# Kernel tuning notes

Measured on AMD Instinct MI355X. Metric: run time of the kernel, lower is better.

Reference implementation:

```python
import jax, jax.numpy as jnp
import numpy as np

M, B, S, D, H = 8, 4, 512, 512, 8
HD = D // H  # head_dim = 64


def setup_inputs() -> dict:
    key = jax.random.key(0)
    k1, k2, k3 = jax.random.split(key, 3)
    x = jax.random.normal(k1, (M, B, S, D), dtype=jnp.float32)
    qkv_weight = jax.random.normal(k2, (M, D, 3 * D), dtype=jnp.float32) * 0.02
    proj_weight = jax.random.normal(k3, (M, D, D), dtype=jnp.float32) * 0.02
    return {"x": x, "qkv_weight": qkv_weight, "proj_weight": proj_weight}


def reference(x, qkv_weight, proj_weight):
    m, b, s, d = x.shape
    # model-axis batched QKV projection
    qkv = jnp.einsum('mbti,mio->mbto', x, qkv_weight)
    q, k, v = jnp.split(qkv, 3, axis=-1)
    # [m, b, h, s, hd]
    q = q.reshape(m, b, s, H, HD).transpose(0, 1, 3, 2, 4)
    k = k.reshape(m, b, s, H, HD).transpose(0, 1, 3, 2, 4)
    v = v.reshape(m, b, s, H, HD).transpose(0, 1, 3, 2, 4)
    att = jnp.einsum('mbhqd,mbhkd->mbhqk', q, k) / jnp.sqrt(jnp.float32(HD))
    causal = jnp.tril(jnp.ones((s, s), dtype=bool))
    att = jnp.where(causal, att, jnp.float32(-jnp.inf))
    att = jax.nn.softmax(att, axis=-1)
    y = jnp.einsum('mbhqk,mbhkd->mbhqd', att, v)
    y = y.transpose(0, 1, 3, 2, 4).reshape(m, b, s, d)
    return jnp.einsum('mbti,mio->mbto', y, proj_weight)
```

## Files before the change

kernel.cpp:

```cpp
#include <hip/hip_runtime.h>
#include <hip/hip_bf16.h>


typedef unsigned short u16;
typedef unsigned int u32;
typedef __attribute__((ext_vector_type(8))) short short8;
typedef __attribute__((ext_vector_type(4))) float f32x4;
typedef __attribute__((ext_vector_type(4))) unsigned short u16x4;
typedef __attribute__((ext_vector_type(8))) unsigned short u16x8;
typedef __attribute__((ext_vector_type(2))) unsigned int u32x2;

#define MFMA16(a, b, c) __builtin_amdgcn_mfma_f32_16x16x32_bf16((a), (b), (c), 0, 0, 0)

__device__ __forceinline__ u16 f2bf(float f) {
  union { __hip_bfloat16 h; u16 u; } cv;
  cv.h = __float2bfloat16(f);
  return cv.u;
}

__device__ __forceinline__ void gl_lds16(const u16* g, u16* l) {
  __builtin_amdgcn_global_load_lds(
      (const __attribute__((address_space(1))) void*)g,
      (__attribute__((address_space(3))) void*)l, 16, 0, 0);
}

__global__ __launch_bounds__(256) void xcast_kernel(const float* __restrict__ in,
                                                    u16* __restrict__ out, long n8) {
  long stride = (long)gridDim.x * 256;
  for (long i = blockIdx.x * 256L + threadIdx.x; i < n8; i += stride) {
    f32x4 a = *(const f32x4*)(in + i * 8);
    f32x4 b = *(const f32x4*)(in + i * 8 + 4);
    u16x8 o = {f2bf(a[0]), f2bf(a[1]), f2bf(a[2]), f2bf(a[3]),
               f2bf(b[0]), f2bf(b[1]), f2bf(b[2]), f2bf(b[3])};
    *(u16x8*)(out + i * 8) = o;
  }
}

__global__ __launch_bounds__(256) void wtrans_kernel(const float* __restrict__ in,
                                                     u16* __restrict__ out, int R, int C) {
  __shared__ float t[32][33];
  int m = blockIdx.z;
  const float* pin = in + (size_t)m * R * C;
  u16* pout = out + (size_t)m * R * C;
  int c0 = blockIdx.x * 32, r0 = blockIdx.y * 32;
  int tx = threadIdx.x, ty = threadIdx.y;
#pragma unroll
  for (int i = 0; i < 4; ++i) {
    int r = ty + i * 8;
    t[r][tx] = pin[(size_t)(r0 + r) * C + c0 + tx];
  }
  __syncthreads();
#pragma unroll
  for (int i = 0; i < 4; ++i) {
    int r = ty + i * 8;
    pout[(size_t)(c0 + r) * R + r0 + tx] = f2bf(t[tx][r]);
  }
}

__global__ __launch_bounds__(256) void qkv_gemm_kernel(const u16* __restrict__ XB,
                                                       const u16* __restrict__ WT,
                                                       u16* __restrict__ Q,
                                                       u16* __restrict__ K,
                                                       u16* __restrict__ VT) {
  __shared__ __attribute__((aligned(16))) u16 As[3][128 * 32];
  __shared__ __attribute__((aligned(16))) u16 Bs[3][128 * 32];
  int bid = blockIdx.x;
  int wgid = (bid & 7) * 192 + (bid >> 3);
  int m = wgid / 192;
  int rem = wgid % 192;
  int r0 = (rem / 12) * 128, c0 = (rem % 12) * 128;
  const u16* A = XB + (size_t)m * 2048 * 512;
  const u16* BT = WT + (size_t)m * 1536 * 512;
  int t = threadIdx.x;
  int lane = t & 63, w = t >> 6;
  int wr = (w >> 1) * 64, wc = (w & 1) * 64;
  int fr = lane & 15, fc = lane >> 4;

  int rA0 = t >> 2, cA0 = t & 3, sA0 = cA0 ^ ((rA0 >> 1) & 3);
  int rA1 = (t + 256) >> 2, cA1 = t & 3, sA1 = cA1 ^ ((rA1 >> 1) & 3);

  f32x4 acc[4][4];
#pragma unroll
  for (int i = 0; i < 4; ++i)
#pragma unroll
    for (int j = 0; j < 4; ++j) acc[i][j] = f32x4{0.f, 0.f, 0.f, 0.f};

#define QKV_STAGE(tile)                                                          \
  {                                                                              \
    int kk_ = (tile) * 32;                                                       \
    int b_ = (tile) % 3;                                                         \
    gl_lds16(A + (size_t)(r0 + rA0) * 512 + kk_ + sA0 * 8, &As[b_][w * 512]);    \
    gl_lds16(A + (size_t)(r0 + rA1) * 512 + kk_ + sA1 * 8, &As[b_][2048 + w * 512]); \
    gl_lds16(BT + (size_t)(c0 + rA0) * 512 + kk_ + sA0 * 8, &Bs[b_][w * 512]);   \
    gl_lds16(BT + (size_t)(c0 + rA1) * 512 + kk_ + sA1 * 8, &Bs[b_][2048 + w * 512]); \
  }

#define QKV_COMPUTE(tile)                                                        \
  {                                                                              \
    int b_ = (tile) % 3;                                                         \
    short8 af[4], bf_[4];                                                        \
    _Pragma("unroll") for (int i = 0; i < 4; ++i) {                              \
      int row = wr + i * 16 + fr;                                                \
      int sl = fc ^ ((row >> 1) & 3);                                            \
      af[i] = *(const short8*)&As[b_][row * 32 + sl * 8];                        \
    }                                                                            \
    _Pragma("unroll") for (int j = 0; j < 4; ++j) {                              \
      int row = wc + j * 16 + fr;                                                \
      int sl = fc ^ ((row >> 1) & 3);                                            \
      bf_[j] = *(const short8*)&Bs[b_][row * 32 + sl * 8];                       \
    }                                                                            \
    _Pragma("unroll") for (int i = 0; i < 4; ++i)                                \
      _Pragma("unroll") for (int j = 0; j < 4; ++j)                              \
        acc[i][j] = MFMA16(af[i], bf_[j], acc[i][j]);                            \
  }

  QKV_STAGE(0);
  QKV_STAGE(1);
  for (int ks = 0; ks < 14; ++ks) {
    asm volatile("s_waitcnt vmcnt(4)" ::: "memory");
    __builtin_amdgcn_sched_barrier(0);
    __builtin_amdgcn_s_barrier();
    QKV_STAGE(ks + 2);
    QKV_COMPUTE(ks);
    __builtin_amdgcn_sched_barrier(0);
  }
  asm volatile("s_waitcnt vmcnt(0)" ::: "memory");
  __builtin_amdgcn_sched_barrier(0);
  __builtin_amdgcn_s_barrier();
  QKV_COMPUTE(14);
  QKV_COMPUTE(15);

  int seg = c0 >> 9;
  if (seg == 2) {
#pragma unroll
    for (int i = 0; i < 4; ++i)
#pragma unroll
      for (int j = 0; j < 4; ++j) {
        int s0 = r0 + wr + i * 16 + fc * 4;
        int gcol = c0 + wc + j * 16 + fr;
        int cc = gcol & 511;
        int hh = cc >> 6, hd = cc & 63;
        int b = s0 >> 9, s = s0 & 511;
        size_t headoff = (size_t)((m * 4 + b) * 8 + hh) * 32768;
        u16x4 pk = {f2bf(acc[i][j][0]), f2bf(acc[i][j][1]),
                    f2bf(acc[i][j][2]), f2bf(acc[i][j][3])};
        *(u16x4*)(VT + headoff + (size_t)hd * 512 + s) = pk;
      }
  } else {
#pragma unroll
    for (int i = 0; i < 4; ++i)
#pragma unroll
      for (int j = 0; j < 4; ++j)
#pragma unroll
        for (int r = 0; r < 4; ++r) {
          int grow = r0 + wr + i * 16 + fc * 4 + r;
          int gcol = c0 + wc + j * 16 + fr;
          int b = grow >> 9, s = grow & 511;
          int cc = gcol & 511;
          int hh = cc >> 6, hd = cc & 63;
          size_t headoff = (size_t)((m * 4 + b) * 8 + hh) * 32768;
          u16 val = f2bf(acc[i][j][r]);
          if (seg == 0) Q[headoff + s * 64 + hd] = val;
          else          K[headoff + s * 64 + hd] = val;
        }
  }
}

__global__ __launch_bounds__(256) void attn_kernel(const u16* __restrict__ Qg,
                                                   const u16* __restrict__ Kg,
                                                   const u16* __restrict__ VTg,
                                                   u16* __restrict__ Yg) {
  __shared__ u16 Ks[2][64][72];
  __shared__ u16 Vs[2][64][72];
  __shared__ u16 Pl[4][16][72];
  int bid = blockIdx.x;
  int qt = bid >> 8;
  int g = bid & 255;
  int h = g & 7, mb = g >> 3;
  int t = threadIdx.x, lane = t & 63, w = t >> 6;
  int fr = lane & 15, fc = lane >> 4;
  size_t hoff = ((size_t)mb * 8 + h) * 32768;
  const u16* Q = Qg + hoff;
  const u16* K = Kg + hoff;
  const u16* V = VTg + hoff;
  int qrow = qt * 64 + w * 16 + fr;
  const float SC = 0.125f * 1.44269504088896340736f;

  short8 qf0 = *(const short8*)(Q + (size_t)qrow * 64 + fc * 8);
  short8 qf1 = *(const short8*)(Q + (size_t)qrow * 64 + 32 + fc * 8);

  f32x4 acc[4];
#pragma unroll
  for (int d = 0; d < 4; ++d) acc[d] = f32x4{0.f, 0.f, 0.f, 0.f};
  float mst = -1e30f, lst = 0.f;

  int u0 = 2 * t, u1 = 2 * t + 1;
  int kr0 = u0 >> 3, kc0 = (u0 & 7) * 8;
  int kr1 = u1 >> 3, kc1 = (u1 & 7) * 8;

  {
    u16x8 a0 = *(const u16x8*)(K + (size_t)kr0 * 64 + kc0);
    u16x8 a1 = *(const u16x8*)(K + (size_t)kr1 * 64 + kc1);
    u16x8 b0 = *(const u16x8*)(V + (size_t)kr0 * 512 + kc0);
    u16x8 b1 = *(const u16x8*)(V + (size_t)kr1 * 512 + kc1);
    *(u16x8*)&Ks[0][kr0][kc0] = a0;
    *(u16x8*)&Ks[0][kr1][kc1] = a1;
    *(u16x8*)&Vs[0][kr0][kc0] = b0;
    *(u16x8*)&Vs[0][kr1][kc1] = b1;
  }
  __syncthreads();

  for (int kt = 0; kt <= qt; ++kt) {
    int cur = kt & 1;
    bool pref = kt < qt;
    u16x8 nk0, nk1, nv0, nv1;
    if (pref) {
      int kbn = (kt + 1) * 64;
      nk0 = *(const u16x8*)(K + (size_t)(kbn + kr0) * 64 + kc0);
      nk1 = *(const u16x8*)(K + (size_t)(kbn + kr1) * 64 + kc1);
      nv0 = *(const u16x8*)(V + (size_t)kr0 * 512 + kbn + kc0);
      nv1 = *(const u16x8*)(V + (size_t)kr1 * 512 + kbn + kc1);
    }

    f32x4 st[4];
#pragma unroll
    for (int sub = 0; sub < 4; ++sub) {
      short8 kf0 = *(const short8*)&Ks[cur][sub * 16 + fr][fc * 8];
      short8 kf1 = *(const short8*)&Ks[cur][sub * 16 + fr][32 + fc * 8];
      f32x4 z = f32x4{0.f, 0.f, 0.f, 0.f};
      z = MFMA16(kf0, qf0, z);
      st[sub] = MFMA16(kf1, qf1, z);
    }

    float p[4][4];
    float mt = -3e30f;
    bool diag = (kt == qt);
    int qloc = w * 16 + fr;
#pragma unroll
    for (int sub = 0; sub < 4; ++sub)
#pragma unroll
      for (int r = 0; r < 4; ++r) {
        float v = st[sub][r] * SC;
        if (diag && (sub * 16 + fc * 4 + r) > qloc) v = -1e30f;
        p[sub][r] = v;
        mt = fmaxf(mt, v);
      }
    mt = fmaxf(mt, __shfl_xor(mt, 16));
    mt = fmaxf(mt, __shfl_xor(mt, 32));
    float mn = fmaxf(mst, mt);
    float al = __builtin_amdgcn_exp2f(mst - mn);
    mst = mn;
    float rs = 0.f;
#pragma unroll
    for (int sub = 0; sub < 4; ++sub)
#pragma unroll
      for (int r = 0; r < 4; ++r) {
        float e = __builtin_amdgcn_exp2f(p[sub][r] - mn);
        p[sub][r] = e;
        rs += e;
      }
    rs += __shfl_xor(rs, 16);
    rs += __shfl_xor(rs, 32);
    lst = lst * al + rs;
#pragma unroll
    for (int d = 0; d < 4; ++d) acc[d] *= al;

#pragma unroll
    for (int sub = 0; sub < 4; ++sub) {
      u32 lo = (u32)f2bf(p[sub][0]) | ((u32)f2bf(p[sub][1]) << 16);
      u32 hi = (u32)f2bf(p[sub][2]) | ((u32)f2bf(p[sub][3]) << 16);
      *(u32x2*)&Pl[w][fr][sub * 16 + fc * 4] = u32x2{lo, hi};
    }

#pragma unroll
    for (int dt = 0; dt < 4; ++dt)
#pragma unroll
      for (int kc = 0; kc < 2; ++kc) {
        short8 vf = *(const short8*)&Vs[cur][dt * 16 + fr][kc * 32 + fc * 8];
        short8 pb = *(const short8*)&Pl[w][fr][kc * 32 + fc * 8];
        acc[dt] = MFMA16(vf, pb, acc[dt]);
      }

    if (pref) {
      *(u16x8*)&Ks[cur ^ 1][kr0][kc0] = nk0;
      *(u16x8*)&Ks[cur ^ 1][kr1][kc1] = nk1;
      *(u16x8*)&Vs[cur ^ 1][kr0][kc0] = nv0;
      *(u16x8*)&Vs[cur ^ 1][kr1][kc1] = nv1;
    }
    __syncthreads();
  }

  float inv = 1.0f / lst;
#pragma unroll
  for (int dt = 0; dt < 4; ++dt) {
    u16x4 o = {f2bf(acc[dt][0] * inv), f2bf(acc[dt][1] * inv),
               f2bf(acc[dt][2] * inv), f2bf(acc[dt][3] * inv)};
    *(u16x4*)(Yg + ((size_t)mb * 512 + qrow) * 512 + h * 64 + dt * 16 + fc * 4) = o;
  }
}

__global__ __launch_bounds__(256) void proj_gemm_kernel(const u16* __restrict__ Y,
                                                        const u16* __restrict__ PT,
                                                        float* __restrict__ OUT) {
  __shared__ __attribute__((aligned(16))) u16 As[3][128 * 32];
  __shared__ __attribute__((aligned(16))) u16 Bs[3][128 * 32];
  int bid = blockIdx.x;
  int wgid = (bid & 7) * 64 + (bid >> 3);
  int m = wgid / 64;
  int rem = wgid % 64;
  int r0 = (rem / 4) * 128, c0 = (rem % 4) * 128;
  const u16* A = Y + (size_t)m * 2048 * 512;
  const u16* BT = PT + (size_t)m * 512 * 512;
  float* C = OUT + (size_t)m * 2048 * 512;
  int t = threadIdx.x;
  int lane = t & 63, w = t >> 6;
  int wr = (w >> 1) * 64, wc = (w & 1) * 64;
  int fr = lane & 15, fc = lane >> 4;

  int rA0 = t >> 2, sA0 = (t & 3) ^ ((rA0 >> 1) & 3);
  int rA1 = (t + 256) >> 2, sA1 = (t & 3) ^ ((rA1 >> 1) & 3);

  f32x4 acc[4][4];
#pragma unroll
  for (int i = 0; i < 4; ++i)
#pragma unroll
    for (int j = 0; j < 4; ++j) acc[i][j] = f32x4{0.f, 0.f, 0.f, 0.f};

#define PROJ_STAGE(tile)                                                         \
  {                                                                              \
    int kk_ = (tile) * 32;                                                       \
    int b_ = (tile) % 3;                                                         \
    gl_lds16(A + (size_t)(r0 + rA0) * 512 + kk_ + sA0 * 8, &As[b_][w * 512]);    \
    gl_lds16(A + (size_t)(r0 + rA1) * 512 + kk_ + sA1 * 8, &As[b_][2048 + w * 512]); \
    gl_lds16(BT + (size_t)(c0 + rA0) * 512 + kk_ + sA0 * 8, &Bs[b_][w * 512]);   \
    gl_lds16(BT + (size_t)(c0 + rA1) * 512 + kk_ + sA1 * 8, &Bs[b_][2048 + w * 512]); \
  }

#define PROJ_COMPUTE(tile)                                                       \
  {                                                                              \
    int b_ = (tile) % 3;                                                         \
    short8 af[4], bf_[4];                                                        \
    _Pragma("unroll") for (int i = 0; i < 4; ++i) {                              \
      int row = wr + i * 16 + fr;                                                \
      int sl = fc ^ ((row >> 1) & 3);                                            \
      af[i] = *(const short8*)&As[b_][row * 32 + sl * 8];                        \
    }                                                                            \
    _Pragma("unroll") for (int j = 0; j < 4; ++j) {                              \
      int row = wc + j * 16 + fr;                                                \
      int sl = fc ^ ((row >> 1) & 3);                                            \
      bf_[j] = *(const short8*)&Bs[b_][row * 32 + sl * 8];                       \
    }                                                                            \
    _Pragma("unroll") for (int i = 0; i < 4; ++i)                                \
      _Pragma("unroll") for (int j = 0; j < 4; ++j)                              \
        acc[i][j] = MFMA16(af[i], bf_[j], acc[i][j]);                            \
  }

  PROJ_STAGE(0);
  PROJ_STAGE(1);
  for (int ks = 0; ks < 14; ++ks) {
    asm volatile("s_waitcnt vmcnt(4)" ::: "memory");
    __builtin_amdgcn_sched_barrier(0);
    __builtin_amdgcn_s_barrier();
    PROJ_STAGE(ks + 2);
    PROJ_COMPUTE(ks);
    __builtin_amdgcn_sched_barrier(0);
  }
  asm volatile("s_waitcnt vmcnt(0)" ::: "memory");
  __builtin_amdgcn_sched_barrier(0);
  __builtin_amdgcn_s_barrier();
  PROJ_COMPUTE(14);
  PROJ_COMPUTE(15);

#pragma unroll
  for (int i = 0; i < 4; ++i)
#pragma unroll
    for (int j = 0; j < 4; ++j)
#pragma unroll
      for (int r = 0; r < 4; ++r) {
        int grow = r0 + wr + i * 16 + fc * 4 + r;
        int gcol = c0 + wc + j * 16 + fr;
        C[(size_t)grow * 512 + gcol] = acc[i][j][r];
      }
}

extern "C" void kernel_launch(void* const* d_in, const int* in_sizes, int n_in,
                              void* d_out, int out_size, void* d_ws, size_t ws_size,
                              hipStream_t stream) {
  const float* x = (const float*)d_in[0];
  const float* wqkv = (const float*)d_in[1];
  const float* wproj = (const float*)d_in[2];
  float* out = (float*)d_out;

  u16* p = (u16*)d_ws;
  u16* wqkvT = p;  p += (size_t)8 * 1536 * 512;
  u16* wprojT = p; p += (size_t)8 * 512 * 512;
  u16* qb = p;     p += (size_t)8388608;
  u16* kb = p;     p += (size_t)8388608;
  u16* vtb = p;    p += (size_t)8388608;
  u16* xyb = p;    p += (size_t)8388608;

  xcast_kernel<<<2048, 256, 0, stream>>>(x, xyb, (long)8 * 4 * 512 * 512 / 8);
  wtrans_kernel<<<dim3(48, 16, 8), dim3(32, 8), 0, stream>>>(wqkv, wqkvT, 512, 1536);
  wtrans_kernel<<<dim3(16, 16, 8), dim3(32, 8), 0, stream>>>(wproj, wprojT, 512, 512);
  qkv_gemm_kernel<<<1536, 256, 0, stream>>>(xyb, wqkvT, qb, kb, vtb);
  attn_kernel<<<2048, 256, 0, stream>>>(qb, kb, vtb, xyb);
  proj_gemm_kernel<<<512, 256, 0, stream>>>(xyb, wprojT, out);
}
```

Baseline: 191.5 us.

## Enlarge GEMM tiles to 256x128 and pair causal query tiles in attention

Both GEMM kernels now run 512-thread workgroups, each computing a 256x128 output tile, so every B tile loaded is reused across twice as many rows and fewer blocks are launched. The attention kernel pairs query tile p with tile 7-p in one block to balance causal work, and shares each K/V tile load between the two. K/V staging now uses asynchronous global-to-LDS loads into an XOR-swizzled layout in place of register round-trips. The trade-off is more registers and LDS per block, which may lower occupancy, and each attention block runs a longer serial loop.

```diff
diff --git a/kernel.cpp b/kernel.cpp
--- a/kernel.cpp
+++ b/kernel.cpp
@@ -57,18 +57,18 @@
   }
 }
 
-__global__ __launch_bounds__(256) void qkv_gemm_kernel(const u16* __restrict__ XB,
+__global__ __launch_bounds__(512) void qkv_gemm_kernel(const u16* __restrict__ XB,
                                                        const u16* __restrict__ WT,
                                                        u16* __restrict__ Q,
                                                        u16* __restrict__ K,
                                                        u16* __restrict__ VT) {
-  __shared__ __attribute__((aligned(16))) u16 As[3][128 * 32];
+  __shared__ __attribute__((aligned(16))) u16 As[3][256 * 32];
   __shared__ __attribute__((aligned(16))) u16 Bs[3][128 * 32];
   int bid = blockIdx.x;
-  int wgid = (bid & 7) * 192 + (bid >> 3);
-  int m = wgid / 192;
-  int rem = wgid % 192;
-  int r0 = (rem / 12) * 128, c0 = (rem % 12) * 128;
+  int wgid = (bid & 7) * 96 + (bid >> 3);
+  int m = wgid / 96;
+  int rem = wgid % 96;
+  int r0 = (rem / 12) * 256, c0 = (rem % 12) * 128;
   const u16* A = XB + (size_t)m * 2048 * 512;
   const u16* BT = WT + (size_t)m * 1536 * 512;
   int t = threadIdx.x;
@@ -76,8 +76,8 @@
   int wr = (w >> 1) * 64, wc = (w & 1) * 64;
   int fr = lane & 15, fc = lane >> 4;
 
-  int rA0 = t >> 2, cA0 = t & 3, sA0 = cA0 ^ ((rA0 >> 1) & 3);
-  int rA1 = (t + 256) >> 2, cA1 = t & 3, sA1 = cA1 ^ ((rA1 >> 1) & 3);
+  int rA0 = t >> 2, sA0 = (t & 3) ^ ((rA0 >> 1) & 3);
+  int rA1 = 128 + (t >> 2), sA1 = (t & 3) ^ ((rA1 >> 1) & 3);
 
   f32x4 acc[4][4];
 #pragma unroll
@@ -85,39 +85,38 @@
 #pragma unroll
     for (int j = 0; j < 4; ++j) acc[i][j] = f32x4{0.f, 0.f, 0.f, 0.f};
 
-#define QKV_STAGE(tile)                                                          \
-  {                                                                              \
-    int kk_ = (tile) * 32;                                                       \
-    int b_ = (tile) % 3;                                                         \
-    gl_lds16(A + (size_t)(r0 + rA0) * 512 + kk_ + sA0 * 8, &As[b_][w * 512]);    \
-    gl_lds16(A + (size_t)(r0 + rA1) * 512 + kk_ + sA1 * 8, &As[b_][2048 + w * 512]); \
-    gl_lds16(BT + (size_t)(c0 + rA0) * 512 + kk_ + sA0 * 8, &Bs[b_][w * 512]);   \
-    gl_lds16(BT + (size_t)(c0 + rA1) * 512 + kk_ + sA1 * 8, &Bs[b_][2048 + w * 512]); \
-  }
-
-#define QKV_COMPUTE(tile)                                                        \
-  {                                                                              \
-    int b_ = (tile) % 3;                                                         \
-    short8 af[4], bf_[4];                                                        \
-    _Pragma("unroll") for (int i = 0; i < 4; ++i) {                              \
-      int row = wr + i * 16 + fr;                                                \
-      int sl = fc ^ ((row >> 1) & 3);                                            \
-      af[i] = *(const short8*)&As[b_][row * 32 + sl * 8];                        \
-    }                                                                            \
-    _Pragma("unroll") for (int j = 0; j < 4; ++j) {                              \
-      int row = wc + j * 16 + fr;                                                \
-      int sl = fc ^ ((row >> 1) & 3);                                            \
-      bf_[j] = *(const short8*)&Bs[b_][row * 32 + sl * 8];                       \
-    }                                                                            \
-    _Pragma("unroll") for (int i = 0; i < 4; ++i)                                \
-      _Pragma("unroll") for (int j = 0; j < 4; ++j)                              \
-        acc[i][j] = MFMA16(af[i], bf_[j], acc[i][j]);                            \
+#define QKV_STAGE(tile)                                                            \
+  {                                                                                \
+    int kk_ = (tile) * 32;                                                         \
+    int b_ = (tile) % 3;                                                           \
+    gl_lds16(A + (size_t)(r0 + rA0) * 512 + kk_ + sA0 * 8, &As[b_][w * 512]);      \
+    gl_lds16(A + (size_t)(r0 + rA1) * 512 + kk_ + sA1 * 8, &As[b_][4096 + w * 512]); \
+    gl_lds16(BT + (size_t)(c0 + rA0) * 512 + kk_ + sA0 * 8, &Bs[b_][w * 512]);     \
+  }
+
+#define QKV_COMPUTE(tile)                                                          \
+  {                                                                                \
+    int b_ = (tile) % 3;                                                           \
+    short8 af[4], bf_[4];                                                          \
+    _Pragma("unroll") for (int i = 0; i < 4; ++i) {                                \
+      int row = wr + i * 16 + fr;                                                  \
+      int sl = fc ^ ((row >> 1) & 3);                                              \
+      af[i] = *(const short8*)&As[b_][row * 32 + sl * 8];                          \
+    }                                                                              \
+    _Pragma("unroll") for (int j = 0; j < 4; ++j) {                                \
+      int row = wc + j * 16 + fr;                                                  \
+      int sl = fc ^ ((row >> 1) & 3);                                              \
+      bf_[j] = *(const short8*)&Bs[b_][row * 32 + sl * 8];                         \
+    }                                                                              \
+    _Pragma("unroll") for (int i = 0; i < 4; ++i)                                  \
+      _Pragma("unroll") for (int j = 0; j < 4; ++j)                                \
+        acc[i][j] = MFMA16(af[i], bf_[j], acc[i][j]);                              \
   }
 
   QKV_STAGE(0);
   QKV_STAGE(1);
   for (int ks = 0; ks < 14; ++ks) {
-    asm volatile("s_waitcnt vmcnt(4)" ::: "memory");
+    asm volatile("s_waitcnt vmcnt(3)" ::: "memory");
     __builtin_amdgcn_sched_barrier(0);
     __builtin_amdgcn_s_barrier();
     QKV_STAGE(ks + 2);
@@ -170,145 +169,153 @@
                                                    const u16* __restrict__ Kg,
                                                    const u16* __restrict__ VTg,
                                                    u16* __restrict__ Yg) {
-  __shared__ u16 Ks[2][64][72];
-  __shared__ u16 Vs[2][64][72];
+  __shared__ __attribute__((aligned(16))) u16 Ks[2][64 * 64];
+  __shared__ __attribute__((aligned(16))) u16 Vs[2][64 * 64];
   __shared__ u16 Pl[4][16][72];
   int bid = blockIdx.x;
-  int qt = bid >> 8;
+  int p = bid >> 8;
   int g = bid & 255;
   int h = g & 7, mb = g >> 3;
+  int qtA = p, qtB = 7 - p;
   int t = threadIdx.x, lane = t & 63, w = t >> 6;
   int fr = lane & 15, fc = lane >> 4;
   size_t hoff = ((size_t)mb * 8 + h) * 32768;
   const u16* Q = Qg + hoff;
   const u16* K = Kg + hoff;
   const u16* V = VTg + hoff;
-  int qrow = qt * 64 + w * 16 + fr;
   const float SC = 0.125f * 1.44269504088896340736f;
 
-  short8 qf0 = *(const short8*)(Q + (size_t)qrow * 64 + fc * 8);
-  short8 qf1 = *(const short8*)(Q + (size_t)qrow * 64 + 32 + fc * 8);
-
-  f32x4 acc[4];
-#pragma unroll
-  for (int d = 0; d < 4; ++d) acc[d] = f32x4{0.f, 0.f, 0.f, 0.f};
-  float mst = -1e30f, lst = 0.f;
-
-  int u0 = 2 * t, u1 = 2 * t + 1;
-  int kr0 = u0 >> 3, kc0 = (u0 & 7) * 8;
-  int kr1 = u1 >> 3, kc1 = (u1 & 7) * 8;
-
-  {
-    u16x8 a0 = *(const u16x8*)(K + (size_t)kr0 * 64 + kc0);
-    u16x8 a1 = *(const u16x8*)(K + (size_t)kr1 * 64 + kc1);
-    u16x8 b0 = *(const u16x8*)(V + (size_t)kr0 * 512 + kc0);
-    u16x8 b1 = *(const u16x8*)(V + (size_t)kr1 * 512 + kc1);
-    *(u16x8*)&Ks[0][kr0][kc0] = a0;
-    *(u16x8*)&Ks[0][kr1][kc1] = a1;
-    *(u16x8*)&Vs[0][kr0][kc0] = b0;
-    *(u16x8*)&Vs[0][kr1][kc1] = b1;
-  }
-  __syncthreads();
-
-  for (int kt = 0; kt <= qt; ++kt) {
+  int qrowA = qtA * 64 + w * 16 + fr;
+  int qrowB = qtB * 64 + w * 16 + fr;
+  short8 qA0 = *(const short8*)(Q + (size_t)qrowA * 64 + fc * 8);
+  short8 qA1 = *(const short8*)(Q + (size_t)qrowA * 64 + 32 + fc * 8);
+  short8 qB0 = *(const short8*)(Q + (size_t)qrowB * 64 + fc * 8);
+  short8 qB1 = *(const short8*)(Q + (size_t)qrowB * 64 + 32 + fc * 8);
+
+  f32x4 accA[4], accB[4];
+#pragma unroll
+  for (int d = 0; d < 4; ++d) {
+    accA[d] = f32x4{0.f, 0.f, 0.f, 0.f};
+    accB[d] = f32x4{0.f, 0.f, 0.f, 0.f};
+  }
+  float mstA = -1e30f, lstA = 0.f, mstB = -1e30f, lstB = 0.f;
+
+  int sr0 = t >> 3, ss0 = (t & 7) ^ (sr0 & 7);
+  int sr1 = 32 + (t >> 3), ss1 = (t & 7) ^ (sr1 & 7);
+
+#define ATTN_STAGE(kt_, buf_)                                                     \
+  {                                                                               \
+    int kb_ = (kt_) * 64;                                                         \
+    gl_lds16(K + (size_t)(kb_ + sr0) * 64 + ss0 * 8, &Ks[buf_][w * 512]);         \
+    gl_lds16(K + (size_t)(kb_ + sr1) * 64 + ss1 * 8, &Ks[buf_][2048 + w * 512]);  \
+    gl_lds16(V + (size_t)sr0 * 512 + kb_ + ss0 * 8, &Vs[buf_][w * 512]);          \
+    gl_lds16(V + (size_t)sr1 * 512 + kb_ + ss1 * 8, &Vs[buf_][2048 + w * 512]);   \
+  }
+
+  int qloc = w * 16 + fr;
+  ATTN_STAGE(0, 0);
+
+  for (int kt = 0; kt <= qtB; ++kt) {
     int cur = kt & 1;
-    bool pref = kt < qt;
-    u16x8 nk0, nk1, nv0, nv1;
-    if (pref) {
-      int kbn = (kt + 1) * 64;
-      nk0 = *(const u16x8*)(K + (size_t)(kbn + kr0) * 64 + kc0);
-      nk1 = *(const u16x8*)(K + (size_t)(kbn + kr1) * 64 + kc1);
-      nv0 = *(const u16x8*)(V + (size_t)kr0 * 512 + kbn + kc0);
-      nv1 = *(const u16x8*)(V + (size_t)kr1 * 512 + kbn + kc1);
+    if (kt < qtB) {
+      ATTN_STAGE(kt + 1, cur ^ 1);
+      asm volatile("s_waitcnt vmcnt(4)" ::: "memory");
+    } else {
+      asm volatile("s_waitcnt vmcnt(0)" ::: "memory");
     }
-
-    f32x4 st[4];
-#pragma unroll
-    for (int sub = 0; sub < 4; ++sub) {
-      short8 kf0 = *(const short8*)&Ks[cur][sub * 16 + fr][fc * 8];
-      short8 kf1 = *(const short8*)&Ks[cur][sub * 16 + fr][32 + fc * 8];
-      f32x4 z = f32x4{0.f, 0.f, 0.f, 0.f};
-      z = MFMA16(kf0, qf0, z);
-      st[sub] = MFMA16(kf1, qf1, z);
-    }
-
-    float p[4][4];
-    float mt = -3e30f;
-    bool diag = (kt == qt);
-    int qloc = w * 16 + fr;
-#pragma unroll
-    for (int sub = 0; sub < 4; ++sub)
-#pragma unroll
-      for (int r = 0; r < 4; ++r) {
-        float v = st[sub][r] * SC;
-        if (diag && (sub * 16 + fc * 4 + r) > qloc) v = -1e30f;
-        p[sub][r] = v;
-        mt = fmaxf(mt, v);
+    __builtin_amdgcn_sched_barrier(0);
+    __builtin_amdgcn_s_barrier();
+
+    auto tile_compute = [&](const short8& qf0, const short8& qf1, f32x4(&acc)[4],
+                            float& mst, float& lst, bool diag) {
+      f32x4 st[4];
+#pragma unroll
+      for (int sub = 0; sub < 4; ++sub) {
+        int row = sub * 16 + fr;
+        short8 kf0 = *(const short8*)&Ks[cur][row * 64 + ((fc ^ (row & 7)) & 7) * 8];
+        short8 kf1 = *(const short8*)&Ks[cur][row * 64 + (((4 + fc) ^ (row & 7)) & 7) * 8];
+        f32x4 z = f32x4{0.f, 0.f, 0.f, 0.f};
+        z = MFMA16(kf0, qf0, z);
+        st[sub] = MFMA16(kf1, qf1, z);
       }
-    mt = fmaxf(mt, __shfl_xor(mt, 16));
-    mt = fmaxf(mt, __shfl_xor(mt, 32));
-    float mn = fmaxf(mst, mt);
-    float al = __builtin_amdgcn_exp2f(mst - mn);
-    mst = mn;
-    float rs = 0.f;
-#pragma unroll
-    for (int sub = 0; sub < 4; ++sub)
-#pragma unroll
-      for (int r = 0; r < 4; ++r) {
-        float e = __builtin_amdgcn_exp2f(p[sub][r] - mn);
-        p[sub][r] = e;
-        rs += e;
+      float pv[4][4];
+      float mt = -3e30f;
+#pragma unroll
+      for (int sub = 0; sub < 4; ++sub)
+#pragma unroll
+        for (int r = 0; r < 4; ++r) {
+          float v = st[sub][r] * SC;
+          if (diag && (sub * 16 + fc * 4 + r) > qloc) v = -1e30f;
+          pv[sub][r] = v;
+          mt = fmaxf(mt, v);
+        }
+      mt = fmaxf(mt, __shfl_xor(mt, 16));
+      mt = fmaxf(mt, __shfl_xor(mt, 32));
+      float mn = fmaxf(mst, mt);
+      float al = __builtin_amdgcn_exp2f(mst - mn);
+      mst = mn;
+      float rs = 0.f;
+#pragma unroll
+      for (int sub = 0; sub < 4; ++sub)
+#pragma unroll
+        for (int r = 0; r < 4; ++r) {
+          float e = __builtin_amdgcn_exp2f(pv[sub][r] - mn);
+          pv[sub][r] = e;
+          rs += e;
+        }
+      rs += __shfl_xor(rs, 16);
+      rs += __shfl_xor(rs, 32);
+      lst = lst * al + rs;
+#pragma unroll
+      for (int d = 0; d < 4; ++d) acc[d] *= al;
+
+#pragma unroll
+      for (int sub = 0; sub < 4; ++sub) {
+        u32 lo = (u32)f2bf(pv[sub][0]) | ((u32)f2bf(pv[sub][1]) << 16);
+        u32 hi = (u32)f2bf(pv[sub][2]) | ((u32)f2bf(pv[sub][3]) << 16);
+        *(u32x2*)&Pl[w][fr][sub * 16 + fc * 4] = u32x2{lo, hi};
       }
-    rs += __shfl_xor(rs, 16);
-    rs += __shfl_xor(rs, 32);
-    lst = lst * al + rs;
-#pragma unroll
-    for (int d = 0; d < 4; ++d) acc[d] *= al;
-
-#pragma unroll
-    for (int sub = 0; sub < 4; ++sub) {
-      u32 lo = (u32)f2bf(p[sub][0]) | ((u32)f2bf(p[sub][1]) << 16);
-      u32 hi = (u32)f2bf(p[sub][2]) | ((u32)f2bf(p[sub][3]) << 16);
-      *(u32x2*)&Pl[w][fr][sub * 16 + fc * 4] = u32x2{lo, hi};
-    }
-
-#pragma unroll
-    for (int dt = 0; dt < 4; ++dt)
-#pragma unroll
-      for (int kc = 0; kc < 2; ++kc) {
-        short8 vf = *(const short8*)&Vs[cur][dt * 16 + fr][kc * 32 + fc * 8];
-        short8 pb = *(const short8*)&Pl[w][fr][kc * 32 + fc * 8];
-        acc[dt] = MFMA16(vf, pb, acc[dt]);
-      }
-
-    if (pref) {
-      *(u16x8*)&Ks[cur ^ 1][kr0][kc0] = nk0;
-      *(u16x8*)&Ks[cur ^ 1][kr1][kc1] = nk1;
-      *(u16x8*)&Vs[cur ^ 1][kr0][kc0] = nv0;
-      *(u16x8*)&Vs[cur ^ 1][kr1][kc1] = nv1;
-    }
-    __syncthreads();
-  }
-
-  float inv = 1.0f / lst;
+#pragma unroll
+      for (int dt = 0; dt < 4; ++dt)
+#pragma unroll
+        for (int kc = 0; kc < 2; ++kc) {
+          int row = dt * 16 + fr;
+          short8 vf = *(const short8*)&Vs[cur][row * 64 + (((kc * 4 + fc) ^ (row & 7)) & 7) * 8];
+          short8 pb = *(const short8*)&Pl[w][fr][kc * 32 + fc * 8];
+          acc[dt] = MFMA16(vf, pb, acc[dt]);
+        }
+    };
+
+    if (kt <= qtA) tile_compute(qA0, qA1, accA, mstA, lstA, kt == qtA);
+    tile_compute(qB0, qB1, accB, mstB, lstB, kt == qtB);
+
+    asm volatile("s_waitcnt lgkmcnt(0)" ::: "memory");
+    __builtin_amdgcn_sched_barrier(0);
+    __builtin_amdgcn_s_barrier();
+  }
+
+  float invA = 1.0f / lstA, invB = 1.0f / lstB;
 #pragma unroll
   for (int dt = 0; dt < 4; ++dt) {
-    u16x4 o = {f2bf(acc[dt][0] * inv), f2bf(acc[dt][1] * inv),
-               f2bf(acc[dt][2] * inv), f2bf(acc[dt][3] * inv)};
-    *(u16x4*)(Yg + ((size_t)mb * 512 + qrow) * 512 + h * 64 + dt * 16 + fc * 4) = o;
-  }
-}
-
-__global__ __launch_bounds__(256) void proj_gemm_kernel(const u16* __restrict__ Y,
+    u16x4 oA = {f2bf(accA[dt][0] * invA), f2bf(accA[dt][1] * invA),
+                f2bf(accA[dt][2] * invA), f2bf(accA[dt][3] * invA)};
+    *(u16x4*)(Yg + ((size_t)mb * 512 + qrowA) * 512 + h * 64 + dt * 16 + fc * 4) = oA;
+    u16x4 oB = {f2bf(accB[dt][0] * invB), f2bf(accB[dt][1] * invB),
+                f2bf(accB[dt][2] * invB), f2bf(accB[dt][3] * invB)};
+    *(u16x4*)(Yg + ((size_t)mb * 512 + qrowB) * 512 + h * 64 + dt * 16 + fc * 4) = oB;
+  }
+}
+
+__global__ __launch_bounds__(512) void proj_gemm_kernel(const u16* __restrict__ Y,
                                                         const u16* __restrict__ PT,
                                                         float* __restrict__ OUT) {
-  __shared__ __attribute__((aligned(16))) u16 As[3][128 * 32];
+  __shared__ __attribute__((aligned(16))) u16 As[3][256 * 32];
   __shared__ __attribute__((aligned(16))) u16 Bs[3][128 * 32];
   int bid = blockIdx.x;
-  int wgid = (bid & 7) * 64 + (bid >> 3);
-  int m = wgid / 64;
-  int rem = wgid % 64;
-  int r0 = (rem / 4) * 128, c0 = (rem % 4) * 128;
+  int wgid = (bid & 7) * 32 + (bid >> 3);
+  int m = wgid / 32;
+  int rem = wgid % 32;
+  int r0 = (rem / 4) * 256, c0 = (rem % 4) * 128;
   const u16* A = Y + (size_t)m * 2048 * 512;
   const u16* BT = PT + (size_t)m * 512 * 512;
   float* C = OUT + (size_t)m * 2048 * 512;
@@ -318,7 +325,7 @@
   int fr = lane & 15, fc = lane >> 4;
 
   int rA0 = t >> 2, sA0 = (t & 3) ^ ((rA0 >> 1) & 3);
-  int rA1 = (t + 256) >> 2, sA1 = (t & 3) ^ ((rA1 >> 1) & 3);
+  int rA1 = 128 + (t >> 2), sA1 = (t & 3) ^ ((rA1 >> 1) & 3);
 
   f32x4 acc[4][4];
 #pragma unroll
@@ -326,39 +333,38 @@
 #pragma unroll
     for (int j = 0; j < 4; ++j) acc[i][j] = f32x4{0.f, 0.f, 0.f, 0.f};
 
-#define PROJ_STAGE(tile)                                                         \
-  {                                                                              \
-    int kk_ = (tile) * 32;                                                       \
-    int b_ = (tile) % 3;                                                         \
-    gl_lds16(A + (size_t)(r0 + rA0) * 512 + kk_ + sA0 * 8, &As[b_][w * 512]);    \
-    gl_lds16(A + (size_t)(r0 + rA1) * 512 + kk_ + sA1 * 8, &As[b_][2048 + w * 512]); \
-    gl_lds16(BT + (size_t)(c0 + rA0) * 512 + kk_ + sA0 * 8, &Bs[b_][w * 512]);   \
-    gl_lds16(BT + (size_t)(c0 + rA1) * 512 + kk_ + sA1 * 8, &Bs[b_][2048 + w * 512]); \
-  }
-
-#define PROJ_COMPUTE(tile)                                                       \
-  {                                                                              \
-    int b_ = (tile) % 3;                                                         \
-    short8 af[4], bf_[4];                                                        \
-    _Pragma("unroll") for (int i = 0; i < 4; ++i) {                              \
-      int row = wr + i * 16 + fr;                                                \
-      int sl = fc ^ ((row >> 1) & 3);                                            \
-      af[i] = *(const short8*)&As[b_][row * 32 + sl * 8];                        \
-    }                                                                            \
-    _Pragma("unroll") for (int j = 0; j < 4; ++j) {                              \
-      int row = wc + j * 16 + fr;                                                \
-      int sl = fc ^ ((row >> 1) & 3);                                            \
-      bf_[j] = *(const short8*)&Bs[b_][row * 32 + sl * 8];                       \
-    }                                                                            \
-    _Pragma("unroll") for (int i = 0; i < 4; ++i)                                \
-      _Pragma("unroll") for (int j = 0; j < 4; ++j)                              \
-        acc[i][j] = MFMA16(af[i], bf_[j], acc[i][j]);                            \
+#define PROJ_STAGE(tile)                                                           \
+  {                                                                                \
+    int kk_ = (tile) * 32;                                                         \
+    int b_ = (tile) % 3;                                                           \
+    gl_lds16(A + (size_t)(r0 + rA0) * 512 + kk_ + sA0 * 8, &As[b_][w * 512]);      \
+    gl_lds16(A + (size_t)(r0 + rA1) * 512 + kk_ + sA1 * 8, &As[b_][4096 + w * 512]); \
+    gl_lds16(BT + (size_t)(c0 + rA0) * 512 + kk_ + sA0 * 8, &Bs[b_][w * 512]);     \
+  }
+
+#define PROJ_COMPUTE(tile)                                                         \
+  {                                                                                \
+    int b_ = (tile) % 3;                                                           \
+    short8 af[4], bf_[4];                                                          \
+    _Pragma("unroll") for (int i = 0; i < 4; ++i) {                                \
+      int row = wr + i * 16 + fr;                                                  \
+      int sl = fc ^ ((row >> 1) & 3);                                              \
+      af[i] = *(const short8*)&As[b_][row * 32 + sl * 8];                          \
+    }                                                                              \
+    _Pragma("unroll") for (int j = 0; j < 4; ++j) {                                \
+      int row = wc + j * 16 + fr;                                                  \
+      int sl = fc ^ ((row >> 1) & 3);                                              \
+      bf_[j] = *(const short8*)&Bs[b_][row * 32 + sl * 8];                         \
+    }                                                                              \
+    _Pragma("unroll") for (int i = 0; i < 4; ++i)                                  \
+      _Pragma("unroll") for (int j = 0; j < 4; ++j)                                \
+        acc[i][j] = MFMA16(af[i], bf_[j], acc[i][j]);                              \
   }
 
   PROJ_STAGE(0);
   PROJ_STAGE(1);
   for (int ks = 0; ks < 14; ++ks) {
-    asm volatile("s_waitcnt vmcnt(4)" ::: "memory");
+    asm volatile("s_waitcnt vmcnt(3)" ::: "memory");
     __builtin_amdgcn_sched_barrier(0);
     __builtin_amdgcn_s_barrier();
     PROJ_STAGE(ks + 2);
@@ -402,7 +408,7 @@
   xcast_kernel<<<2048, 256, 0, stream>>>(x, xyb, (long)8 * 4 * 512 * 512 / 8);
   wtrans_kernel<<<dim3(48, 16, 8), dim3(32, 8), 0, stream>>>(wqkv, wqkvT, 512, 1536);
   wtrans_kernel<<<dim3(16, 16, 8), dim3(32, 8), 0, stream>>>(wproj, wprojT, 512, 512);
-  qkv_gemm_kernel<<<1536, 256, 0, stream>>>(xyb, wqkvT, qb, kb, vtb);
-  attn_kernel<<<2048, 256, 0, stream>>>(qb, kb, vtb, xyb);
-  proj_gemm_kernel<<<512, 256, 0, stream>>>(xyb, wprojT, out);
-}
+  qkv_gemm_kernel<<<768, 512, 0, stream>>>(xyb, wqkvT, qb, kb, vtb);
+  attn_kernel<<<1024, 256, 0, stream>>>(qb, kb, vtb, xyb);
+  proj_gemm_kernel<<<256, 512, 0, stream>>>(xyb, wprojT, out);
+}
```

New measurement: 190.4 us. No clear change (-0.6%).
